# Kernel tuning notes

Hardware: AMD Instinct MI355X
Metric: run time of the kernel (lower is better)

## Reference

```python
import jax, jax.numpy as jnp
import numpy as np

B, N, H, NH = 8, 1024, 512, 8
DK = H // NH


def setup_inputs() -> dict:
    key = jax.random.key(0)
    ks = jax.random.split(key, 6)
    x = jax.random.normal(ks[0], (B, N, H), dtype=jnp.float32)
    adj = jax.random.randint(ks[1], (B, N, N), 0, 2, dtype=jnp.int32)
    # ensure no all-zero row (self-loops) so softmax is well-defined
    adj = jnp.maximum(adj, jnp.eye(N, dtype=jnp.int32)[None])
    s = 1.0 / np.sqrt(H)
    Wq = jax.random.normal(ks[2], (H, H), dtype=jnp.float32) * s
    Wk = jax.random.normal(ks[3], (H, H), dtype=jnp.float32) * s
    Wv = jax.random.normal(ks[4], (H, H), dtype=jnp.float32) * s
    Wg = jax.random.normal(ks[5], (H, 2 * H), dtype=jnp.float32) * (1.0 / np.sqrt(2 * H))
    bg = jnp.zeros((H,), dtype=jnp.float32)
    return {"x": x, "adj": adj, "Wq": Wq, "Wk": Wk, "Wv": Wv, "Wg": Wg, "bg": bg}


def reference(x, adj, Wq, Wk, Wv, Wg, bg):
    b, n, h = x.shape
    # projections (nn.Linear: x @ W.T), split heads -> [b, n, nh, dk]
    q = (x @ Wq.T).reshape(b, n, NH, DK)
    k = (x @ Wk.T).reshape(b, n, NH, DK)
    v = (x @ Wv.T).reshape(b, n, NH, DK)
    # scaled masked attention: [b, nh, n, n]
    scores = jnp.einsum('bqhd,bkhd->bhqk', q, k) / jnp.sqrt(jnp.float32(DK))
    mask = (adj != 0)[:, None, :, :]
    scores = jnp.where(mask, scores, -jnp.inf)
    attn = jax.nn.softmax(scores, axis=-1)  # dropout p=0.0 -> identity
    c = jnp.einsum('bhqk,bkhd->bqhd', attn, v).reshape(b, n, h)
    # sigmoid gated residual combine
    gate = jax.nn.sigmoid(jnp.concatenate([c, x], axis=2) @ Wg.T + bg)
    return gate * x + (1.0 - gate) * c
```

## Files before the change

### kernel.cpp

```cpp
#include <hip/hip_runtime.h>
#include <math.h>

#define B_  8
#define N_  1024
#define H_  512
#define NH_ 8
#define DK_ 64
#define M_  (B_ * N_)

typedef __attribute__((ext_vector_type(4))) float f32x4;
typedef __attribute__((ext_vector_type(8))) short bf16x8;

__device__ __forceinline__ unsigned short f2bf(float f) {
    unsigned int u = __float_as_uint(f);
    u = (u + 0x7fffu + ((u >> 16) & 1u)) >> 16;
    return (unsigned short)u;
}

__device__ __forceinline__ float bf2f(unsigned short s) {
    return __uint_as_float(((unsigned int)s) << 16);
}

__device__ __forceinline__ float fexp2(float x) {
#if __has_builtin(__builtin_amdgcn_exp2f)
    return __builtin_amdgcn_exp2f(x);
#else
    return exp2f(x);
#endif
}

__device__ __forceinline__ void gload16(const unsigned short* g, unsigned short* l) {
    __builtin_amdgcn_global_load_lds(
        (const __attribute__((address_space(1))) void*)g,
        (__attribute__((address_space(3))) void*)l, 16, 0, 0);
}

__global__ __launch_bounds__(256) void prep_k(const float* __restrict__ x,
                                              const float* __restrict__ Wq,
                                              const float* __restrict__ Wk,
                                              const float* __restrict__ Wv,
                                              const float* __restrict__ Wg,
                                              const int*   __restrict__ adj,
                                              unsigned short* __restrict__ xb,
                                              unsigned short* __restrict__ wqb,
                                              unsigned short* __restrict__ wkb,
                                              unsigned short* __restrict__ wvb,
                                              unsigned short* __restrict__ wgb,
                                              unsigned long long* __restrict__ mb)
{
    int id = blockIdx.x;
    if (id >= 5376) {
        int row  = id - 5376;
        int wv   = threadIdx.x >> 6;
        int lane = threadIdx.x & 63;
        const int* arow = &adj[(size_t)row * N_];
        #pragma unroll
        for (int j = 0; j < 4; ++j) {
            int kt = wv * 4 + j;
            int val = arow[kt * 64 + lane];
            unsigned long long m = __ballot(val != 0);
            if (lane == 0) mb[(size_t)row * 16 + kt] = m;
        }
        return;
    }
    const float* src; unsigned short* dst; int off; float scale = 1.0f;
    if (id < 4096)      { src = x;  dst = xb;  off = id; }
    else if (id < 4352) { src = Wq; dst = wqb; off = id - 4096; scale = 0.18033688011112042f; }
    else if (id < 4608) { src = Wk; dst = wkb; off = id - 4352; }
    else if (id < 4864) { src = Wv; dst = wvb; off = id - 4608; }
    else                { src = Wg; dst = wgb; off = id - 4864; }
    size_t i = (size_t)off * 1024 + threadIdx.x * 4;
    float4 v = *(const float4*)&src[i];
    *(ushort4*)&dst[i] = make_ushort4(f2bf(v.x * scale), f2bf(v.y * scale),
                                      f2bf(v.z * scale), f2bf(v.w * scale));
}

__global__ __launch_bounds__(256, 3) void proj_k(const unsigned short* __restrict__ xb,
                                                 const unsigned short* __restrict__ Wqb,
                                                 const unsigned short* __restrict__ Wkb,
                                                 const unsigned short* __restrict__ Wvb,
                                                 unsigned short* __restrict__ qk,
                                                 unsigned short* __restrict__ vt)
{
    __shared__ __align__(16) unsigned short SMEM[24576];

    const int tid = threadIdx.x;
    const int lane = tid & 63, wv = tid >> 6;
    const int ln = lane & 15, quad = lane >> 4;
    const int wm = wv >> 1, wn = wv & 1;
    const int row0 = blockIdx.x * 128;
    const int w    = blockIdx.y >> 2;
    const int col0 = (blockIdx.y & 3) * 128;
    const unsigned short* W = (w == 0) ? Wqb : ((w == 1) ? Wkb : Wvb);
    f32x4 acc[4][4] = {};

    auto issue = [&](int t, int bi) {
        int kt = t * 32;
        #pragma unroll
        for (int i = 0; i < 2; ++i) {
            int c = tid + i * 256;
            int c4 = c >> 7, row = c & 127;
            gload16(&xb[(size_t)(row0 + row) * H_ + kt + c4 * 8], &SMEM[bi * 8192 + c * 8]);
            gload16(&W [(size_t)(col0 + row) * H_ + kt + c4 * 8], &SMEM[bi * 8192 + 4096 + c * 8]);
        }
    };

    issue(0, 0);
    issue(1, 1);
    for (int t = 0; t < 16; ++t) {
        if (t < 15) { asm volatile("s_waitcnt vmcnt(4)" ::: "memory"); }
        else        { asm volatile("s_waitcnt vmcnt(0)" ::: "memory"); }
        __builtin_amdgcn_s_barrier();
        __builtin_amdgcn_sched_barrier(0);
        if (t < 14) issue(t + 2, (t + 2) % 3);
        const unsigned short* Ac = &SMEM[(t % 3) * 8192];
        const unsigned short* Bc = Ac + 4096;
        bf16x8 af[4], bf[4];
        #pragma unroll
        for (int u = 0; u < 4; ++u) {
            af[u] = *(const bf16x8*)&Ac[(quad * 128 + wm * 64 + u * 16 + ln) * 8];
            bf[u] = *(const bf16x8*)&Bc[(quad * 128 + wn * 64 + u * 16 + ln) * 8];
        }
        #pragma unroll
        for (int mt = 0; mt < 4; ++mt)
            #pragma unroll
            for (int nt = 0; nt < 4; ++nt)
                acc[mt][nt] = __builtin_amdgcn_mfma_f32_16x16x32_bf16(af[mt], bf[nt], acc[mt][nt], 0, 0, 0);
    }

    if (w < 2) {
        __syncthreads();
        unsigned short* Ts = SMEM;
        #pragma unroll
        for (int mt = 0; mt < 4; ++mt)
            #pragma unroll
            for (int nt = 0; nt < 4; ++nt)
                #pragma unroll
                for (int r = 0; r < 4; ++r) {
                    int m_local = wm * 64 + mt * 16 + quad * 4 + r;
                    int c_local = wn * 64 + nt * 16 + ln;
                    Ts[m_local * 136 + c_local] = f2bf(acc[mt][nt][r]);
                }
        __syncthreads();
        #pragma unroll
        for (int j = 0; j < 8; ++j) {
            int m = j * 16 + (tid >> 4);
            int c = (tid & 15) * 8;
            uint4 u = *(const uint4*)&Ts[m * 136 + c];
            *(uint4*)&qk[(size_t)(row0 + m) * (2 * H_) + w * H_ + col0 + c] = u;
        }
    } else {
        __syncthreads();
        unsigned short* Ts = SMEM;
        #pragma unroll
        for (int mt = 0; mt < 4; ++mt)
            #pragma unroll
            for (int nt = 0; nt < 4; ++nt) {
                int c_local = wn * 64 + nt * 16 + ln;
                int n_local = wm * 64 + mt * 16 + quad * 4;
                ushort4 u = make_ushort4(f2bf(acc[mt][nt][0]), f2bf(acc[mt][nt][1]),
                                         f2bf(acc[mt][nt][2]), f2bf(acc[mt][nt][3]));
                *(ushort4*)&Ts[c_local * 136 + n_local] = u;
            }
        __syncthreads();
        const int bb = row0 >> 10, n_base = row0 & (N_ - 1);
        #pragma unroll
        for (int j = 0; j < 8; ++j) {
            int c_local = (tid >> 4) + j * 16;
            int nc = (tid & 15) * 8;
            int cg = col0 + c_local;
            int head = cg >> 6, d = cg & 63;
            uint4 u = *(const uint4*)&Ts[c_local * 136 + nc];
            *(uint4*)&vt[((size_t)(bb * NH_ + head) * DK_ + d) * N_ + n_base + nc] = u;
        }
    }
}

__global__ __launch_bounds__(256, 2) void attn_k(const unsigned short* __restrict__ qk,
                                                 const unsigned short* __restrict__ Vt,
                                                 const unsigned long long* __restrict__ Mb,
                                                 unsigned short* __restrict__ Cmb)
{
    const int bh   = blockIdx.x & 63;
    const int qt   = blockIdx.x >> 6;
    const int b    = bh >> 3;
    const int head = bh & 7;

    __shared__ unsigned short Ks[3][4096];
    __shared__ unsigned short Vs[3][4096];
    __shared__ unsigned short Ps[4][2][16][72];

    const int tid = threadIdx.x;
    const int lane = tid & 63, wv = tid >> 6;
    const int ln = lane & 15, quad = lane >> 4;
    const int q0 = qt * 128 + wv * 32 + ln;
    const int q1 = q0 + 16;

    const unsigned short* Kbase = qk + H_ + head * DK_;
    const unsigned short* Vbase = Vt + (size_t)(b * NH_ + head) * DK_ * N_;

    bf16x8 bq[2][2];
    #pragma unroll
    for (int kk = 0; kk < 2; ++kk) {
        bq[0][kk] = *(const bf16x8*)&qk[(size_t)(b * N_ + q0) * (2 * H_) + head * DK_ + kk * 32 + quad * 8];
        bq[1][kk] = *(const bf16x8*)&qk[(size_t)(b * N_ + q1) * (2 * H_) + head * DK_ + kk * 32 + quad * 8];
    }

    bf16x8 ones;
    #pragma unroll
    for (int j = 0; j < 8; ++j) ones[j] = (short)0x3F80;

    f32x4 o[2][4] = {};
    f32x4 osum[2] = {};

    auto issue = [&](int t, int bi) {
        #pragma unroll
        for (int i = 0; i < 2; ++i) {
            int c = tid + i * 256;
            int c8 = c >> 6, row = c & 63;
            gload16(&Kbase[(size_t)(b * N_ + t * 64 + row) * (2 * H_) + c8 * 8], &Ks[bi][c * 8]);
            gload16(&Vbase[(size_t)row * N_ + t * 64 + c8 * 8], &Vs[bi][c * 8]);
        }
    };

    issue(0, 0);
    issue(1, 1);

    for (int t = 0; t < 16; ++t) {
        if (t < 15) { asm volatile("s_waitcnt vmcnt(4)" ::: "memory"); }
        else        { asm volatile("s_waitcnt vmcnt(0)" ::: "memory"); }
        __builtin_amdgcn_s_barrier();
        __builtin_amdgcn_sched_barrier(0);

        unsigned long long mq[2];
        mq[0] = Mb[(size_t)(b * N_ + q0) * 16 + t];
        mq[1] = Mb[(size_t)(b * N_ + q1) * 16 + t];

        if (t < 14) issue(t + 2, (t + 2) % 3);
        const unsigned short* Kc = Ks[t % 3];
        const unsigned short* Vc = Vs[t % 3];

        f32x4 s[2][4] = {};
        __builtin_amdgcn_s_setprio(1);
        #pragma unroll
        for (int kk = 0; kk < 2; ++kk)
            #pragma unroll
            for (int nt = 0; nt < 4; ++nt) {
                bf16x8 ka = *(const bf16x8*)&Kc[((kk * 4 + quad) * 64 + nt * 16 + ln) * 8];
                s[0][nt] = __builtin_amdgcn_mfma_f32_16x16x32_bf16(ka, bq[0][kk], s[0][nt], 0, 0, 0);
                s[1][nt] = __builtin_amdgcn_mfma_f32_16x16x32_bf16(ka, bq[1][kk], s[1][nt], 0, 0, 0);
            }
        __builtin_amdgcn_s_setprio(0);

        #pragma unroll
        for (int g = 0; g < 2; ++g) {
            unsigned long long sh = mq[g] >> (quad * 4);
            #pragma unroll
            for (int nt = 0; nt < 4; ++nt) {
                unsigned int bn = (unsigned int)(sh >> (nt * 16)) & 0xFu;
                float p[4];
                #pragma unroll
                for (int r = 0; r < 4; ++r) {
                    float e = fexp2(s[g][nt][r]);
                    p[r] = (bn & (1u << r)) ? e : 0.f;
                }
                unsigned int d0 = __builtin_amdgcn_perm(__float_as_uint(p[1]), __float_as_uint(p[0]), 0x07060302u);
                unsigned int d1 = __builtin_amdgcn_perm(__float_as_uint(p[3]), __float_as_uint(p[2]), 0x07060302u);
                *(uint2*)&Ps[wv][g][ln][nt * 16 + quad * 4] = make_uint2(d0, d1);
            }
        }

        bf16x8 pb[2][2];
        #pragma unroll
        for (int g = 0; g < 2; ++g)
            #pragma unroll
            for (int kk = 0; kk < 2; ++kk)
                pb[g][kk] = *(const bf16x8*)&Ps[wv][g][ln][kk * 32 + quad * 8];

        __builtin_amdgcn_s_setprio(1);
        #pragma unroll
        for (int kk = 0; kk < 2; ++kk) {
            #pragma unroll
            for (int dt = 0; dt < 4; ++dt) {
                bf16x8 va = *(const bf16x8*)&Vc[((kk * 4 + quad) * 64 + dt * 16 + ln) * 8];
                o[0][dt] = __builtin_amdgcn_mfma_f32_16x16x32_bf16(va, pb[0][kk], o[0][dt], 0, 0, 0);
                o[1][dt] = __builtin_amdgcn_mfma_f32_16x16x32_bf16(va, pb[1][kk], o[1][dt], 0, 0, 0);
            }
            osum[0] = __builtin_amdgcn_mfma_f32_16x16x32_bf16(ones, pb[0][kk], osum[0], 0, 0, 0);
            osum[1] = __builtin_amdgcn_mfma_f32_16x16x32_bf16(ones, pb[1][kk], osum[1], 0, 0, 0);
        }
        __builtin_amdgcn_s_setprio(0);
    }

    #pragma unroll
    for (int g = 0; g < 2; ++g) {
        float inv = 1.f / osum[g][0];
        int qg = (g == 0) ? q0 : q1;
        #pragma unroll
        for (int dt = 0; dt < 4; ++dt) {
            ushort4 u = make_ushort4(f2bf(o[g][dt][0] * inv), f2bf(o[g][dt][1] * inv),
                                     f2bf(o[g][dt][2] * inv), f2bf(o[g][dt][3] * inv));
            *(ushort4*)&Cmb[(size_t)(b * N_ + qg) * H_ + head * DK_ + dt * 16 + quad * 4] = u;
        }
    }
}

__global__ __launch_bounds__(256, 2) void gate_k(const unsigned short* __restrict__ cmb,
                                                 const unsigned short* __restrict__ xb,
                                                 const unsigned short* __restrict__ Wgb,
                                                 const float* __restrict__ bgp,
                                                 float* __restrict__ out)
{
    __shared__ __align__(16) unsigned short GSM[36864];
    const int tid = threadIdx.x;
    const int lane = tid & 63, wv = tid >> 6;
    const int ln = lane & 15, quad = lane >> 4;
    const int wm = wv >> 1, wn = wv & 1;
    const int row0 = blockIdx.x * 128;
    const int col0 = blockIdx.y * 64;
    f32x4 acc[4][2] = {};

    auto issue = [&](int t, int bi) {
        const unsigned short* Asrc = (t < 8) ? cmb : xb;
        int ko = (t * 64) & (H_ - 1);
        #pragma unroll
        for (int i = 0; i < 4; ++i) {
            int c = tid + i * 256;
            int c8 = c >> 7, row = c & 127;
            gload16(&Asrc[(size_t)(row0 + row) * H_ + ko + c8 * 8], &GSM[bi * 12288 + c * 8]);
        }
        #pragma unroll
        for (int i = 0; i < 2; ++i) {
            int c = tid + i * 256;
            int c8 = c >> 6, row = c & 63;
            gload16(&Wgb[(size_t)(col0 + row) * (2 * H_) + t * 64 + c8 * 8], &GSM[bi * 12288 + 8192 + c * 8]);
        }
    };

    issue(0, 0);
    issue(1, 1);
    for (int t = 0; t < 16; ++t) {
        if (t < 15) { asm volatile("s_waitcnt vmcnt(6)" ::: "memory"); }
        else        { asm volatile("s_waitcnt vmcnt(0)" ::: "memory"); }
        __builtin_amdgcn_s_barrier();
        __builtin_amdgcn_sched_barrier(0);
        if (t < 14) issue(t + 2, (t + 2) % 3);
        const unsigned short* Ac = &GSM[(t % 3) * 12288];
        const unsigned short* Bc = Ac + 8192;
        #pragma unroll
        for (int kk = 0; kk < 2; ++kk) {
            bf16x8 af[4], bf[2];
            #pragma unroll
            for (int u = 0; u < 4; ++u)
                af[u] = *(const bf16x8*)&Ac[((kk * 4 + quad) * 128 + wm * 64 + u * 16 + ln) * 8];
            #pragma unroll
            for (int u = 0; u < 2; ++u)
                bf[u] = *(const bf16x8*)&Bc[((kk * 4 + quad) * 64 + wn * 32 + u * 16 + ln) * 8];
            #pragma unroll
            for (int mt = 0; mt < 4; ++mt)
                #pragma unroll
                for (int nt = 0; nt < 2; ++nt)
                    acc[mt][nt] = __builtin_amdgcn_mfma_f32_16x16x32_bf16(af[mt], bf[nt], acc[mt][nt], 0, 0, 0);
        }
    }

    __syncthreads();
    float* Tsf = (float*)GSM;
    #pragma unroll
    for (int mt = 0; mt < 4; ++mt)
        #pragma unroll
        for (int nt = 0; nt < 2; ++nt)
            #pragma unroll
            for (int r = 0; r < 4; ++r) {
                int m_local = wm * 64 + mt * 16 + quad * 4 + r;
                int c_local = wn * 32 + nt * 16 + ln;
                Tsf[m_local * 68 + c_local] = acc[mt][nt][r];
            }
    __syncthreads();

    const int cl = (tid & 15) * 4;
    const float4 bg4 = *(const float4*)&bgp[col0 + cl];
    #pragma unroll
    for (int j = 0; j < 8; ++j) {
        int m = j * 16 + (tid >> 4);
        f32x4 a = *(const f32x4*)&Tsf[m * 68 + cl];
        ushort4 xv4 = *(const ushort4*)&xb [(size_t)(row0 + m) * H_ + col0 + cl];
        ushort4 cv4 = *(const ushort4*)&cmb[(size_t)(row0 + m) * H_ + col0 + cl];
        float4 o;
        {
            float g0 = 1.f / (1.f + __expf(-(a[0] + bg4.x)));
            float g1 = 1.f / (1.f + __expf(-(a[1] + bg4.y)));
            float g2 = 1.f / (1.f + __expf(-(a[2] + bg4.z)));
            float g3 = 1.f / (1.f + __expf(-(a[3] + bg4.w)));
            o.x = g0 * bf2f(xv4.x) + (1.f - g0) * bf2f(cv4.x);
            o.y = g1 * bf2f(xv4.y) + (1.f - g1) * bf2f(cv4.y);
            o.z = g2 * bf2f(xv4.z) + (1.f - g2) * bf2f(cv4.z);
            o.w = g3 * bf2f(xv4.w) + (1.f - g3) * bf2f(cv4.w);
        }
        *(float4*)&out[(size_t)(row0 + m) * H_ + col0 + cl] = o;
    }
}

extern "C" void kernel_launch(void* const* d_in, const int* in_sizes, int n_in,
                              void* d_out, int out_size, void* d_ws, size_t ws_size,
                              hipStream_t stream)
{
    const float* x   = (const float*)d_in[0];
    const int*   adj = (const int*)  d_in[1];
    const float* Wq  = (const float*)d_in[2];
    const float* Wk  = (const float*)d_in[3];
    const float* Wv  = (const float*)d_in[4];
    const float* Wg  = (const float*)d_in[5];
    const float* bg  = (const float*)d_in[6];
    float* out = (float*)d_out;

    unsigned short* xb  = (unsigned short*)d_ws;
    unsigned short* wqb = xb  + (size_t)M_ * H_;
    unsigned short* wkb = wqb + (size_t)H_ * H_;
    unsigned short* wvb = wkb + (size_t)H_ * H_;
    unsigned short* wgb = wvb + (size_t)H_ * H_;
    unsigned short* qk  = wgb + (size_t)H_ * 2 * H_;
    unsigned short* vt  = qk  + (size_t)M_ * 2 * H_;
    unsigned short* cmb = vt  + (size_t)M_ * H_;
    unsigned long long* mb = (unsigned long long*)(cmb + (size_t)M_ * H_);

    prep_k<<<5376 + 8192, 256, 0, stream>>>(x, Wq, Wk, Wv, Wg, adj,
                                            xb, wqb, wkb, wvb, wgb, mb);

    proj_k<<<dim3(M_ / 128, 12), 256, 0, stream>>>(xb, wqb, wkb, wvb, qk, vt);

    attn_k<<<B_ * NH_ * (N_ / 128), 256, 0, stream>>>(qk, vt, mb, cmb);

    gate_k<<<dim3(M_ / 128, H_ / 64), 256, 0, stream>>>(cmb, xb, wgb, bg, out);
}
```

Measured before the change: 196.2 us.

## Split attention block across 8 waves and stage mask bits via LDS async loads

The attention kernel now runs 512 threads per block, so each wave handles 16 query rows instead of 32, which halves per-wave accumulator registers and raises the occupancy target. The mask words are prefetched asynchronously into LDS with global_load_lds, double-buffered per pair of key tiles, instead of being loaded directly from global memory inside the loop. The loop is unrolled by two to fit the new vmcnt accounting. This trades more K/V LDS reads per query row and more barrier participants for better latency hiding.

```diff
diff --git a/kernel.cpp b/kernel.cpp
--- a/kernel.cpp
+++ b/kernel.cpp
@@ -176,7 +176,7 @@
     }
 }
 
-__global__ __launch_bounds__(256, 2) void attn_k(const unsigned short* __restrict__ qk,
+__global__ __launch_bounds__(512, 4) void attn_k(const unsigned short* __restrict__ qk,
                                                  const unsigned short* __restrict__ Vt,
                                                  const unsigned long long* __restrict__ Mb,
                                                  unsigned short* __restrict__ Cmb)
@@ -186,96 +186,80 @@
     const int b    = bh >> 3;
     const int head = bh & 7;
 
-    __shared__ unsigned short Ks[3][4096];
-    __shared__ unsigned short Vs[3][4096];
-    __shared__ unsigned short Ps[4][2][16][72];
+    __shared__ __align__(16) unsigned short Ks[3][4096];
+    __shared__ __align__(16) unsigned short Vs[3][4096];
+    __shared__ __align__(16) unsigned short Ps[8][16][72];
+    __shared__ __align__(16) unsigned long long Ms[2][8][16][2];
 
     const int tid = threadIdx.x;
     const int lane = tid & 63, wv = tid >> 6;
     const int ln = lane & 15, quad = lane >> 4;
-    const int q0 = qt * 128 + wv * 32 + ln;
-    const int q1 = q0 + 16;
+    const int q0 = qt * 128 + wv * 16 + ln;
 
     const unsigned short* Kbase = qk + H_ + head * DK_;
     const unsigned short* Vbase = Vt + (size_t)(b * NH_ + head) * DK_ * N_;
 
-    bf16x8 bq[2][2];
+    bf16x8 bq[2];
     #pragma unroll
-    for (int kk = 0; kk < 2; ++kk) {
-        bq[0][kk] = *(const bf16x8*)&qk[(size_t)(b * N_ + q0) * (2 * H_) + head * DK_ + kk * 32 + quad * 8];
-        bq[1][kk] = *(const bf16x8*)&qk[(size_t)(b * N_ + q1) * (2 * H_) + head * DK_ + kk * 32 + quad * 8];
-    }
+    for (int kk = 0; kk < 2; ++kk)
+        bq[kk] = *(const bf16x8*)&qk[(size_t)(b * N_ + q0) * (2 * H_) + head * DK_ + kk * 32 + quad * 8];
 
     bf16x8 ones;
     #pragma unroll
     for (int j = 0; j < 8; ++j) ones[j] = (short)0x3F80;
 
-    f32x4 o[2][4] = {};
-    f32x4 osum[2] = {};
+    f32x4 o[4] = {};
+    f32x4 osum = {};
 
     auto issue = [&](int t, int bi) {
-        #pragma unroll
-        for (int i = 0; i < 2; ++i) {
-            int c = tid + i * 256;
-            int c8 = c >> 6, row = c & 63;
-            gload16(&Kbase[(size_t)(b * N_ + t * 64 + row) * (2 * H_) + c8 * 8], &Ks[bi][c * 8]);
-            gload16(&Vbase[(size_t)row * N_ + t * 64 + c8 * 8], &Vs[bi][c * 8]);
-        }
+        gload16(&Kbase[(size_t)(b * N_ + t * 64 + lane) * (2 * H_) + wv * 8], &Ks[bi][tid * 8]);
+        gload16(&Vbase[(size_t)lane * N_ + t * 64 + wv * 8], &Vs[bi][tid * 8]);
     };
-
-    issue(0, 0);
-    issue(1, 1);
-
-    for (int t = 0; t < 16; ++t) {
-        if (t < 15) { asm volatile("s_waitcnt vmcnt(4)" ::: "memory"); }
-        else        { asm volatile("s_waitcnt vmcnt(0)" ::: "memory"); }
-        __builtin_amdgcn_s_barrier();
-        __builtin_amdgcn_sched_barrier(0);
-
-        unsigned long long mq[2];
-        mq[0] = Mb[(size_t)(b * N_ + q0) * 16 + t];
-        mq[1] = Mb[(size_t)(b * N_ + q1) * 16 + t];
-
-        if (t < 14) issue(t + 2, (t + 2) % 3);
+    auto mask_issue = [&](int tp, int pb) {
+        if (lane < 16) {
+            const unsigned long long* src =
+                &Mb[(size_t)(b * N_ + qt * 128 + wv * 16 + lane) * 16 + tp * 2];
+            __builtin_amdgcn_global_load_lds(
+                (const __attribute__((address_space(1))) void*)src,
+                (__attribute__((address_space(3))) void*)&Ms[pb][wv][lane][0], 16, 0, 0);
+        }
+    };
+
+    auto compute = [&](int t, int tp) {
         const unsigned short* Kc = Ks[t % 3];
         const unsigned short* Vc = Vs[t % 3];
-
-        f32x4 s[2][4] = {};
+        unsigned long long mq = Ms[tp & 1][wv][ln][t & 1];
+
+        f32x4 s[4] = {};
         __builtin_amdgcn_s_setprio(1);
         #pragma unroll
         for (int kk = 0; kk < 2; ++kk)
             #pragma unroll
             for (int nt = 0; nt < 4; ++nt) {
                 bf16x8 ka = *(const bf16x8*)&Kc[((kk * 4 + quad) * 64 + nt * 16 + ln) * 8];
-                s[0][nt] = __builtin_amdgcn_mfma_f32_16x16x32_bf16(ka, bq[0][kk], s[0][nt], 0, 0, 0);
-                s[1][nt] = __builtin_amdgcn_mfma_f32_16x16x32_bf16(ka, bq[1][kk], s[1][nt], 0, 0, 0);
+                s[nt] = __builtin_amdgcn_mfma_f32_16x16x32_bf16(ka, bq[kk], s[nt], 0, 0, 0);
             }
         __builtin_amdgcn_s_setprio(0);
 
-        #pragma unroll
-        for (int g = 0; g < 2; ++g) {
-            unsigned long long sh = mq[g] >> (quad * 4);
-            #pragma unroll
-            for (int nt = 0; nt < 4; ++nt) {
-                unsigned int bn = (unsigned int)(sh >> (nt * 16)) & 0xFu;
-                float p[4];
-                #pragma unroll
-                for (int r = 0; r < 4; ++r) {
-                    float e = fexp2(s[g][nt][r]);
-                    p[r] = (bn & (1u << r)) ? e : 0.f;
-                }
-                unsigned int d0 = __builtin_amdgcn_perm(__float_as_uint(p[1]), __float_as_uint(p[0]), 0x07060302u);
-                unsigned int d1 = __builtin_amdgcn_perm(__float_as_uint(p[3]), __float_as_uint(p[2]), 0x07060302u);
-                *(uint2*)&Ps[wv][g][ln][nt * 16 + quad * 4] = make_uint2(d0, d1);
+        unsigned long long sh = mq >> (quad * 4);
+        #pragma unroll
+        for (int nt = 0; nt < 4; ++nt) {
+            unsigned int bn = (unsigned int)(sh >> (nt * 16)) & 0xFu;
+            float p[4];
+            #pragma unroll
+            for (int r = 0; r < 4; ++r) {
+                float e = fexp2(s[nt][r]);
+                p[r] = (bn & (1u << r)) ? e : 0.f;
             }
-        }
-
-        bf16x8 pb[2][2];
-        #pragma unroll
-        for (int g = 0; g < 2; ++g)
-            #pragma unroll
-            for (int kk = 0; kk < 2; ++kk)
-                pb[g][kk] = *(const bf16x8*)&Ps[wv][g][ln][kk * 32 + quad * 8];
+            unsigned int d0 = __builtin_amdgcn_perm(__float_as_uint(p[1]), __float_as_uint(p[0]), 0x07060302u);
+            unsigned int d1 = __builtin_amdgcn_perm(__float_as_uint(p[3]), __float_as_uint(p[2]), 0x07060302u);
+            *(uint2*)&Ps[wv][ln][nt * 16 + quad * 4] = make_uint2(d0, d1);
+        }
+
+        bf16x8 pb[2];
+        #pragma unroll
+        for (int kk = 0; kk < 2; ++kk)
+            pb[kk] = *(const bf16x8*)&Ps[wv][ln][kk * 32 + quad * 8];
 
         __builtin_amdgcn_s_setprio(1);
         #pragma unroll
@@ -283,25 +267,43 @@
             #pragma unroll
             for (int dt = 0; dt < 4; ++dt) {
                 bf16x8 va = *(const bf16x8*)&Vc[((kk * 4 + quad) * 64 + dt * 16 + ln) * 8];
-                o[0][dt] = __builtin_amdgcn_mfma_f32_16x16x32_bf16(va, pb[0][kk], o[0][dt], 0, 0, 0);
-                o[1][dt] = __builtin_amdgcn_mfma_f32_16x16x32_bf16(va, pb[1][kk], o[1][dt], 0, 0, 0);
+                o[dt] = __builtin_amdgcn_mfma_f32_16x16x32_bf16(va, pb[kk], o[dt], 0, 0, 0);
             }
-            osum[0] = __builtin_amdgcn_mfma_f32_16x16x32_bf16(ones, pb[0][kk], osum[0], 0, 0, 0);
-            osum[1] = __builtin_amdgcn_mfma_f32_16x16x32_bf16(ones, pb[1][kk], osum[1], 0, 0, 0);
+            osum = __builtin_amdgcn_mfma_f32_16x16x32_bf16(ones, pb[kk], osum, 0, 0, 0);
         }
         __builtin_amdgcn_s_setprio(0);
-    }
-
+    };
+
+    issue(0, 0);
+    mask_issue(0, 0);
+    issue(1, 1);
+
+    for (int tp = 0; tp < 8; ++tp) {
+        {
+            const int t = 2 * tp;
+            asm volatile("s_waitcnt vmcnt(2)" ::: "memory");
+            __builtin_amdgcn_s_barrier();
+            __builtin_amdgcn_sched_barrier(0);
+            if (t < 14) { issue(t + 2, (t + 2) % 3); mask_issue(tp + 1, (tp + 1) & 1); }
+            compute(t, tp);
+        }
+        {
+            const int t = 2 * tp + 1;
+            if (tp < 7) { asm volatile("s_waitcnt vmcnt(3)" ::: "memory"); }
+            else        { asm volatile("s_waitcnt vmcnt(0)" ::: "memory"); }
+            __builtin_amdgcn_s_barrier();
+            __builtin_amdgcn_sched_barrier(0);
+            if (t < 14) issue(t + 2, (t + 2) % 3);
+            compute(t, tp);
+        }
+    }
+
+    float inv = 1.f / osum[0];
     #pragma unroll
-    for (int g = 0; g < 2; ++g) {
-        float inv = 1.f / osum[g][0];
-        int qg = (g == 0) ? q0 : q1;
-        #pragma unroll
-        for (int dt = 0; dt < 4; ++dt) {
-            ushort4 u = make_ushort4(f2bf(o[g][dt][0] * inv), f2bf(o[g][dt][1] * inv),
-                                     f2bf(o[g][dt][2] * inv), f2bf(o[g][dt][3] * inv));
-            *(ushort4*)&Cmb[(size_t)(b * N_ + qg) * H_ + head * DK_ + dt * 16 + quad * 4] = u;
-        }
+    for (int dt = 0; dt < 4; ++dt) {
+        ushort4 u = make_ushort4(f2bf(o[dt][0] * inv), f2bf(o[dt][1] * inv),
+                                 f2bf(o[dt][2] * inv), f2bf(o[dt][3] * inv));
+        *(ushort4*)&Cmb[(size_t)(b * N_ + q0) * H_ + head * DK_ + dt * 16 + quad * 4] = u;
     }
 }
 
@@ -429,7 +431,7 @@
 
     proj_k<<<dim3(M_ / 128, 12), 256, 0, stream>>>(xb, wqb, wkb, wvb, qk, vt);
 
-    attn_k<<<B_ * NH_ * (N_ / 128), 256, 0, stream>>>(qk, vt, mb, cmb);
+    attn_k<<<B_ * NH_ * (N_ / 128), 512, 0, stream>>>(qk, vt, mb, cmb);
 
     gate_k<<<dim3(M_ / 128, H_ / 64), 256, 0, stream>>>(cmb, xb, wgb, bg, out);
 }
```

Result: no change. 194.6 us (-0.8%).
